# Performance work log

Measured on AMD Instinct MI355X. Metric: run time of the kernel, lower is better.

Reference implementation:

```python
import jax, jax.numpy as jnp
import numpy as np

# static config (matches init_kwargs)
WS = (8, 7, 7)       # window size (T, H, W)
SS = (4, 3, 3)       # shift size (T, H, W)
NUM_HEADS = 4
B, T, H, W, C = 2, 16, 56, 56, 128
VOL = WS[0] * WS[1] * WS[2]  # 392 tokens per window


def _compute_attention_mask_3d(size_dhw, window_size, shift_size):
    """Static numpy replica of torch _compute_attention_mask_3d -> [nW, V, V]."""
    m = np.zeros(size_dhw, dtype=np.float32)
    slices = [((0, -window_size[i]), (-window_size[i], -shift_size[i]), (-shift_size[i], None))
              for i in range(3)]
    cnt = 0
    for d0, d1 in slices[0]:
        for h0, h1 in slices[1]:
            for w0, w1 in slices[2]:
                m[d0:d1, h0:h1, w0:w1] = cnt
                cnt += 1
    nT, nH, nW_ = (size_dhw[0] // window_size[0], size_dhw[1] // window_size[1],
                   size_dhw[2] // window_size[2])
    m = m.reshape(nT, window_size[0], nH, window_size[1], nW_, window_size[2])
    m = m.transpose(0, 2, 4, 1, 3, 5).reshape(nT * nH * nW_, VOL)
    diff = m[:, None, :] - m[:, :, None]
    return np.where(diff != 0, np.float32(-100.0), np.float32(0.0))


_ATTN_MASK = jnp.asarray(_compute_attention_mask_3d((T, H, W), WS, SS))  # [nW, V, V]


def setup_inputs() -> dict:
    key = jax.random.key(0)
    ks = jax.random.split(key, 6)
    s = 0.02
    return {
        "x": jax.random.normal(ks[0], (B, T, H, W, C), jnp.float32),
        "qkv_weight": jax.random.normal(ks[1], (3 * C, C), jnp.float32) * s,
        "qkv_bias": jax.random.normal(ks[2], (3 * C,), jnp.float32) * s,
        "proj_weight": jax.random.normal(ks[3], (C, C), jnp.float32) * s,
        "proj_bias": jax.random.normal(ks[4], (C,), jnp.float32) * s,
        "rel_pos_bias": jax.random.normal(ks[5], (1, NUM_HEADS, VOL, VOL), jnp.float32) * s,
    }


def reference(x, qkv_weight, qkv_bias, proj_weight, proj_bias, rel_pos_bias):
    b, t, h, w, c = x.shape
    hd = c // NUM_HEADS
    wt, wh, ww = WS
    nt, nh, nw = t // wt, h // wh, w // ww
    n_win = nt * nh * nw

    # cyclic shift (T,H,W divide the window so no padding needed)
    xs = jnp.roll(x, shift=(-SS[0], -SS[1], -SS[2]), axis=(1, 2, 3))

    # window partition -> [b*n_win, VOL, c]
    xw = xs.reshape(b, nt, wt, nh, wh, nw, ww, c)
    xw = xw.transpose(0, 1, 3, 5, 2, 4, 6, 7).reshape(b * n_win, VOL, c)

    # qkv projection
    qkv = xw @ qkv_weight.T + qkv_bias
    qkv = qkv.reshape(b * n_win, VOL, 3, NUM_HEADS, hd).transpose(2, 0, 3, 1, 4)
    q, k, v = qkv[0], qkv[1], qkv[2]          # [b*nW, nH, V, hd]
    q = q * (hd ** -0.5)

    attn = jnp.einsum("whqd,whkd->whqk", q, k) + rel_pos_bias
    # shift mask: broadcast over batch and heads
    attn = attn.reshape(b, n_win, NUM_HEADS, VOL, VOL) + _ATTN_MASK[None, :, None, :, :]
    attn = jax.nn.softmax(attn.reshape(b * n_win, NUM_HEADS, VOL, VOL), axis=-1)

    out = jnp.einsum("whqk,whkd->whqd", attn, v)         # [b*nW, nH, V, hd]
    out = out.transpose(0, 2, 1, 3).reshape(b * n_win, VOL, c)
    out = out @ proj_weight.T + proj_bias

    # window un-partition -> [b, t, h, w, c]
    out = out.reshape(b, nt, nh, nw, wt, wh, ww, c)
    out = out.transpose(0, 1, 4, 2, 5, 3, 6, 7).reshape(b, t, h, w, c)
    out = jnp.roll(out, shift=(SS[0], SS[1], SS[2]), axis=(1, 2, 3))
    return out
```

## Files before the change

### kernel.cpp

```cpp
#include <hip/hip_runtime.h>
#include <hip/hip_bf16.h>

typedef __bf16 bf16;
typedef __bf16 bf16x4 __attribute__((ext_vector_type(4)));
typedef __bf16 bf16x8 __attribute__((ext_vector_type(8)));
typedef float f32x4 __attribute__((ext_vector_type(4)));

#define MFMA(a, b, c) __builtin_amdgcn_mfma_f32_16x16x32_bf16(a, b, c, 0, 0, 0)

__device__ inline f32x4 zf4() { return f32x4{0.f, 0.f, 0.f, 0.f}; }

constexpr int Tc = 16, Hc = 56, Wc = 56, Cc = 128, NHc = 4, HDc = 32;
constexpr int VOL = 392;
constexpr int STc = 4, SHc = 3, SWc = 3;
constexpr int TWIN = 256;
constexpr int MTOT = TWIN * VOL;
constexpr int QSZ = TWIN * NHc * VOL * HDc;
constexpr int BMT_N = 8 * 4 * 400 * 416;

__device__ inline bf16x8 zero8() {
    bf16x8 z;
#pragma unroll
    for (int j = 0; j < 8; ++j) z[j] = (bf16)0.0f;
    return z;
}

__device__ inline f32x4 up4(bf16x4 b) {
    f32x4 r;
#pragma unroll
    for (int j = 0; j < 4; ++j) r[j] = (float)b[j];
    return r;
}

__device__ inline int cls_of(int v, int pt, int ph, int pw) {
    int tt = v / 49, rem = v % 49, hh = rem / 7, ww = rem % 7;
    int ct = pt ? (tt < 4 ? 1 : 2) : 0;
    int ch = ph ? (hh < 4 ? 1 : 2) : 0;
    int cw = pw ? (ww < 4 ? 1 : 2) : 0;
    return ct * 9 + ch * 3 + cw;
}

__global__ void prep_kernel(const float* __restrict__ wq, const float* __restrict__ bq,
                            const float* __restrict__ wp, const float* __restrict__ bp,
                            const float* __restrict__ rpb,
                            bf16* __restrict__ wqb, bf16* __restrict__ bqb,
                            bf16* __restrict__ wpb, bf16* __restrict__ bpb,
                            bf16* __restrict__ bmt) {
    const int blk = blockIdx.x, tid = threadIdx.x;
    if (blk < 65) {
        int i = blk * 256 + tid;
        const float* s; bf16* d; int off;
        if (i < 12288)       { s = wq; d = wqb; off = i; }
        else if (i < 12384)  { s = bq; d = bqb; off = i - 12288; }
        else if (i < 16480)  { s = wp; d = wpb; off = i - 12384; }
        else if (i < 16512)  { s = bp; d = bpb; off = i - 16480; }
        else return;
        f32x4 v = *(const f32x4*)(s + (size_t)off * 4);
        bf16x4 o;
#pragma unroll
        for (int j = 0; j < 4; ++j) o[j] = (bf16)v[j];
        *(bf16x4*)(d + (size_t)off * 4) = o;
        return;
    }
    __shared__ unsigned char clsc[392];
    int bb = blk - 65;
    int pat = bb / 100, rem = bb % 100;
    int head = rem / 25, rc = rem % 25;
    int pt = (pat >> 2) & 1, ph = (pat >> 1) & 1, pw = pat & 1;
    for (int v = tid; v < 392; v += 256) clsc[v] = (unsigned char)cls_of(v, pt, ph, pw);
    __syncthreads();
    bf16* dst = bmt + ((size_t)(pat * NHc + head) * 400 + rc * 16) * 416;
    for (int idx = tid; idx < 16 * 104; idx += 256) {
        int lr = idx / 104, c4 = idx % 104;
        int row = rc * 16 + lr;
        bf16x4 o;
        if (row >= VOL) {
#pragma unroll
            for (int j = 0; j < 4; ++j) o[j] = (bf16)0.f;
        } else {
            int rcls = clsc[row];
            const float* brow = rpb + (size_t)(head * VOL + row) * VOL;
#pragma unroll
            for (int j = 0; j < 4; ++j) {
                int col = c4 * 4 + j;
                float v;
                if (col >= VOL) v = -144.0f;
                else {
                    v = brow[col] * 1.4426950408889634f;
                    if (clsc[col] != rcls) v -= 144.0f;
                }
                o[j] = (bf16)v;
            }
        }
        *(bf16x4*)(dst + (size_t)lr * 416 + c4 * 4) = o;
    }
}

__global__ __launch_bounds__(256, 3)
void qkv_kernel(const float* __restrict__ x, const bf16* __restrict__ wq,
                const bf16* __restrict__ bq, bf16* __restrict__ qws,
                bf16* __restrict__ kws, bf16* __restrict__ vws) {
    __shared__ bf16 As[64][136];
    __shared__ bf16 Cs[64][204];
    __shared__ unsigned int rb[64];
    __shared__ unsigned int rbw[64];
    const int tid = threadIdx.x;
    const int m0 = blockIdx.x * 64;

    if (tid < 64) {
        int g = m0 + tid;
        int win = g / VOL, tok = g % VOL;
        int b = win >> 7, wi = win & 127;
        int wt_i = wi >> 6, wh_i = (wi >> 3) & 7, ww_i = wi & 7;
        int tt = tok / 49, r2 = tok % 49, hh = r2 / 7, ww2 = r2 % 7;
        int t = wt_i * 8 + tt + STc; if (t >= Tc) t -= Tc;
        int h = wh_i * 7 + hh + SHc; if (h >= Hc) h -= Hc;
        int w = ww_i * 7 + ww2 + SWc; if (w >= Wc) w -= Wc;
        rb[tid] = (unsigned int)((((b * Tc + t) * Hc + h) * Wc + w) * Cc * 4);
        rbw[tid] = (unsigned int)((win << 9) | tok);
    }
    __syncthreads();

    for (int idx = tid; idx < 64 * 32; idx += 256) {
        int r = idx >> 5, c = idx & 31;
        const float* src = (const float*)((const char*)x + rb[r]) + c * 4;
        f32x4 v = *(const f32x4*)src;
        bf16x4 o;
#pragma unroll
        for (int j = 0; j < 4; ++j) o[j] = (bf16)v[j];
        *(bf16x4*)(&As[r][c * 4]) = o;
    }
    __syncthreads();

    const int wid = tid >> 6, lane = tid & 63;
    const int quad = lane >> 4, l15 = lane & 15;
    const int nbase = wid * 96;

    f32x4 acc[6][4];
#pragma unroll
    for (int mt = 0; mt < 6; ++mt)
#pragma unroll
        for (int nt = 0; nt < 4; ++nt) acc[mt][nt] = zf4();

#pragma unroll
    for (int ko = 0; ko < 4; ++ko) {
        bf16x8 xf[4];
#pragma unroll
        for (int nt = 0; nt < 4; ++nt)
            xf[nt] = *(const bf16x8*)(&As[nt * 16 + l15][ko * 32 + quad * 8]);
#pragma unroll
        for (int mt = 0; mt < 6; ++mt) {
            bf16x8 wf = *(const bf16x8*)(wq + (size_t)(nbase + mt * 16 + l15) * Cc + ko * 32 + quad * 8);
#pragma unroll
            for (int nt = 0; nt < 4; ++nt)
                acc[mt][nt] = MFMA(wf, xf[nt], acc[mt][nt]);
        }
    }

#pragma unroll 1
    for (int phase = 0; phase < 2; ++phase) {
        if ((wid >> 1) == phase) {
#pragma unroll
            for (int mt = 0; mt < 6; ++mt) {
                int colbase = nbase + mt * 16 + quad * 4;
                int lc = colbase - phase * 192;
                bf16x4 bc = *(const bf16x4*)(bq + colbase);
                float scale = (colbase < 128) ? 0.25505653942f : 1.0f;
#pragma unroll
                for (int nt = 0; nt < 4; ++nt) {
                    bf16x4 o;
#pragma unroll
                    for (int r = 0; r < 4; ++r)
                        o[r] = (bf16)((acc[mt][nt][r] + (float)bc[r]) * scale);
                    *(bf16x4*)(&Cs[nt * 16 + l15][lc]) = o;
                }
            }
        }
        __syncthreads();
        for (int u = tid; u < 64 * 6; u += 256) {
            int row = u / 6, s = u - row * 6;
            int gs = phase * 6 + s;
            bf16* basep = (gs < 4) ? qws : (gs < 8) ? kws : vws;
            int head = gs & 3;
            unsigned int p = rbw[row];
            int win = p >> 9, tok = p & 511;
            size_t off = ((size_t)(win * NHc + head) * VOL + tok) * HDc;
#pragma unroll
            for (int c = 0; c < 4; ++c) {
                bf16x4 lo = *(const bf16x4*)(&Cs[row][s * 32 + c * 8]);
                bf16x4 hi = *(const bf16x4*)(&Cs[row][s * 32 + c * 8 + 4]);
                *(bf16x8*)(basep + off + c * 8) = __builtin_shufflevector(lo, hi, 0, 1, 2, 3, 4, 5, 6, 7);
            }
        }
        __syncthreads();
    }
}

__global__ __launch_bounds__(512, 4)
void attn_kernel(const bf16* __restrict__ qws, const bf16* __restrict__ kws,
                 const bf16* __restrict__ vws, const bf16* __restrict__ bmt,
                 bf16* __restrict__ aows) {
    __shared__ bf16 Kl[400][40];
    __shared__ bf16 Vt[32][424];
    __shared__ bf16 Pb[8][2][16][40];

    const int tid = threadIdx.x;
    const int win = blockIdx.x >> 2, head = blockIdx.x & 3;
    const int wi = win & 127;
    const int wt_i = wi >> 6, wh_i = (wi >> 3) & 7, ww_i = wi & 7;
    const int pat = ((wt_i == 1) << 2) | ((wh_i == 7) << 1) | (ww_i == 7);

    const bf16* Qg = qws + (size_t)(win * NHc + head) * VOL * HDc;
    const bf16* Kg = kws + (size_t)(win * NHc + head) * VOL * HDc;
    const bf16* Vg = vws + (size_t)(win * NHc + head) * VOL * HDc;
    const bf16* Bg = bmt + (size_t)(pat * NHc + head) * 400 * 416;

    for (int idx = tid; idx < 400 * 4; idx += 512) {
        int tok = idx >> 2, c = idx & 3;
        bf16x8 v = zero8();
        if (tok < VOL) v = *(const bf16x8*)(Kg + tok * HDc + c * 8);
        *(bf16x8*)(&Kl[tok][c * 8]) = v;
    }
    if (tid < 416) {
        int c = tid & 3, tok4 = (tid >> 2) * 4;
        bf16x8 rr[4];
#pragma unroll
        for (int i = 0; i < 4; ++i)
            rr[i] = (tok4 + i < VOL) ? *(const bf16x8*)(Vg + (tok4 + i) * HDc + c * 8) : zero8();
#pragma unroll
        for (int j = 0; j < 8; ++j) {
            bf16x4 wv;
            wv[0] = rr[0][j]; wv[1] = rr[1][j]; wv[2] = rr[2][j]; wv[3] = rr[3][j];
            *(bf16x4*)(&Vt[c * 8 + j][tok4]) = wv;
        }
    }
    __syncthreads();

    const int wid = tid >> 6, lane = tid & 63;
    const int quad = lane >> 4, l15 = lane & 15;
    bf16* PwA = &Pb[wid][0][0][0];
    bf16* PwB = &Pb[wid][1][0][0];

    for (int pass = 0; pass < 2; ++pass) {
        const int qtA = pass * 16 + wid, qtB = qtA + 8;
        const bool hasB = (qtB < 25);
        const int qbA = qtA * 16, qbB = qtB * 16;
        int qrA = qbA + l15; if (qrA >= VOL) qrA = VOL - 1;
        const bf16x8 qfA = *(const bf16x8*)(Qg + (size_t)qrA * HDc + quad * 8);
        const bf16* BrA = Bg + (size_t)(qbA + l15) * 416;
        const bf16* BrB = BrA;
        bf16x8 qfB;
        if (hasB) {
            int qrB = qbB + l15; if (qrB >= VOL) qrB = VOL - 1;
            qfB = *(const bf16x8*)(Qg + (size_t)qrB * HDc + quad * 8);
            BrB = Bg + (size_t)(qbB + l15) * 416;
        }
        f32x4 oA0 = zf4(), oA1 = zf4(), oB0 = zf4(), oB1 = zf4();
        float lsA = 0.f, lsB = 0.f;
        bf16x4 nbA0 = *(const bf16x4*)(BrA + quad * 4);
        bf16x4 nbA1 = *(const bf16x4*)(BrA + 16 + quad * 4);
        bf16x4 nbB0, nbB1;
        if (hasB) {
            nbB0 = *(const bf16x4*)(BrB + quad * 4);
            nbB1 = *(const bf16x4*)(BrB + 16 + quad * 4);
        }

        bf16x8 kc0 = *(const bf16x8*)(&Kl[l15][quad * 8]);
        bf16x8 kc1 = *(const bf16x8*)(&Kl[16 + l15][quad * 8]);
        bf16x8 vc0 = *(const bf16x8*)(&Vt[l15][quad * 8]);
        bf16x8 vc1 = *(const bf16x8*)(&Vt[16 + l15][quad * 8]);

        auto qk_full = [&](int kb) {
            bf16x8 kn0, kn1;
            if (kb < 384) {
                kn0 = *(const bf16x8*)(&Kl[kb + 32 + l15][quad * 8]);
                kn1 = *(const bf16x8*)(&Kl[kb + 48 + l15][quad * 8]);
            }
            f32x4 cA0 = up4(nbA0), cA1 = up4(nbA1), cB0, cB1;
            if (hasB) { cB0 = up4(nbB0); cB1 = up4(nbB1); }
            if (kb < 384) {
                nbA0 = *(const bf16x4*)(BrA + kb + 32 + quad * 4);
                nbA1 = *(const bf16x4*)(BrA + kb + 48 + quad * 4);
                if (hasB) {
                    nbB0 = *(const bf16x4*)(BrB + kb + 32 + quad * 4);
                    nbB1 = *(const bf16x4*)(BrB + kb + 48 + quad * 4);
                }
            }
            f32x4 sA0 = MFMA(kc0, qfA, cA0);
            f32x4 sA1 = MFMA(kc1, qfA, cA1);
            bf16x4 pA0, pA1;
            float la = 0.f;
#pragma unroll
            for (int r = 0; r < 4; ++r) {
                float e0 = __builtin_amdgcn_exp2f(sA0[r]);
                float e1 = __builtin_amdgcn_exp2f(sA1[r]);
                pA0[r] = (bf16)e0; pA1[r] = (bf16)e1; la += e0 + e1;
            }
            lsA += la;
            *(bf16x4*)(PwA + l15 * 40 + quad * 4) = pA0;
            *(bf16x4*)(PwA + l15 * 40 + 16 + quad * 4) = pA1;
            if (hasB) {
                f32x4 sB0 = MFMA(kc0, qfB, cB0);
                f32x4 sB1 = MFMA(kc1, qfB, cB1);
                bf16x4 pB0, pB1;
                float lb = 0.f;
#pragma unroll
                for (int r = 0; r < 4; ++r) {
                    float e0 = __builtin_amdgcn_exp2f(sB0[r]);
                    float e1 = __builtin_amdgcn_exp2f(sB1[r]);
                    pB0[r] = (bf16)e0; pB1[r] = (bf16)e1; lb += e0 + e1;
                }
                lsB += lb;
                *(bf16x4*)(PwB + l15 * 40 + quad * 4) = pB0;
                *(bf16x4*)(PwB + l15 * 40 + 16 + quad * 4) = pB1;
            }
            kc0 = kn0; kc1 = kn1;
        };
        auto pv = [&](int kb) {
            bf16x8 pfA = *(const bf16x8*)(PwA + l15 * 40 + quad * 8);
            bf16x8 pfB;
            if (hasB) pfB = *(const bf16x8*)(PwB + l15 * 40 + quad * 8);
            bf16x8 vn0, vn1;
            if (kb < 384) {
                vn0 = *(const bf16x8*)(&Vt[l15][kb + 32 + quad * 8]);
                vn1 = *(const bf16x8*)(&Vt[16 + l15][kb + 32 + quad * 8]);
            }
            oA0 = MFMA(vc0, pfA, oA0);
            oA1 = MFMA(vc1, pfA, oA1);
            if (hasB) { oB0 = MFMA(vc0, pfB, oB0); oB1 = MFMA(vc1, pfB, oB1); }
            vc0 = vn0; vc1 = vn1;
        };

        qk_full(0);
#pragma unroll 1
        for (int kt = 1; kt < 12; ++kt) {
            pv((kt - 1) * 32);
            qk_full(kt * 32);
        }
        pv(352);
        {
            f32x4 cA0 = up4(nbA0), cB0;
            if (hasB) cB0 = up4(nbB0);
            f32x4 sA0 = MFMA(kc0, qfA, cA0);
            bf16x4 pA0, z4;
            float la = 0.f;
#pragma unroll
            for (int r = 0; r < 4; ++r) {
                float e0 = __builtin_amdgcn_exp2f(sA0[r]);
                pA0[r] = (bf16)e0; la += e0; z4[r] = (bf16)0.f;
            }
            lsA += la;
            *(bf16x4*)(PwA + l15 * 40 + quad * 4) = pA0;
            *(bf16x4*)(PwA + l15 * 40 + 16 + quad * 4) = z4;
            if (hasB) {
                f32x4 sB0 = MFMA(kc0, qfB, cB0);
                bf16x4 pB0;
                float lb = 0.f;
#pragma unroll
                for (int r = 0; r < 4; ++r) {
                    float e0 = __builtin_amdgcn_exp2f(sB0[r]);
                    pB0[r] = (bf16)e0; lb += e0;
                }
                lsB += lb;
                *(bf16x4*)(PwB + l15 * 40 + quad * 4) = pB0;
                *(bf16x4*)(PwB + l15 * 40 + 16 + quad * 4) = z4;
            }
        }
        pv(384);

        lsA += __shfl_xor(lsA, 16); lsA += __shfl_xor(lsA, 32);
        if (hasB) { lsB += __shfl_xor(lsB, 16); lsB += __shfl_xor(lsB, 32); }
        if (qbA + l15 < VOL) {
            float inv = 1.f / lsA;
            bf16x4 w0, w1;
#pragma unroll
            for (int r = 0; r < 4; ++r) { w0[r] = (bf16)(oA0[r] * inv); w1[r] = (bf16)(oA1[r] * inv); }
            bf16* dst = aows + ((size_t)win * VOL + qbA + l15) * Cc + head * HDc;
            *(bf16x4*)(dst + quad * 4) = w0;
            *(bf16x4*)(dst + 16 + quad * 4) = w1;
        }
        if (hasB && qbB + l15 < VOL) {
            float inv = 1.f / lsB;
            bf16x4 w0, w1;
#pragma unroll
            for (int r = 0; r < 4; ++r) { w0[r] = (bf16)(oB0[r] * inv); w1[r] = (bf16)(oB1[r] * inv); }
            bf16* dst = aows + ((size_t)win * VOL + qbB + l15) * Cc + head * HDc;
            *(bf16x4*)(dst + quad * 4) = w0;
            *(bf16x4*)(dst + 16 + quad * 4) = w1;
        }
    }
}

__global__ __launch_bounds__(256, 2)
void proj_kernel(const bf16* __restrict__ aows, const bf16* __restrict__ wp,
                 const bf16* __restrict__ bp, float* __restrict__ out) {
    __shared__ bf16 As[64][136];
    __shared__ float Csf[64][132];
    __shared__ unsigned int rbo[64];
    const int tid = threadIdx.x;
    const int m0 = blockIdx.x * 64;

    if (tid < 64) {
        int g = m0 + tid;
        int win = g / VOL, tok = g % VOL;
        int b = win >> 7, wi = win & 127;
        int wt_i = wi >> 6, wh_i = (wi >> 3) & 7, ww_i = wi & 7;
        int tt = tok / 49, r2 = tok % 49, hh = r2 / 7, ww2 = r2 % 7;
        int t = wt_i * 8 + tt + STc; if (t >= Tc) t -= Tc;
        int h = wh_i * 7 + hh + SHc; if (h >= Hc) h -= Hc;
        int w = ww_i * 7 + ww2 + SWc; if (w >= Wc) w -= Wc;
        rbo[tid] = (unsigned int)((((b * Tc + t) * Hc + h) * Wc + w) * Cc * 4);
    }
    for (int idx = tid; idx < 64 * 16; idx += 256) {
        int r = idx >> 4, c = idx & 15;
        *(bf16x8*)(&As[r][c * 8]) = *(const bf16x8*)(aows + (size_t)(m0 + r) * Cc + c * 8);
    }
    __syncthreads();

    const int wid = tid >> 6, lane = tid & 63;
    const int quad = lane >> 4, l15 = lane & 15;

    f32x4 acc[8];
#pragma unroll
    for (int mt = 0; mt < 8; ++mt) acc[mt] = zf4();

#pragma unroll
    for (int ko = 0; ko < 4; ++ko) {
        bf16x8 xf = *(const bf16x8*)(&As[wid * 16 + l15][ko * 32 + quad * 8]);
#pragma unroll
        for (int mt = 0; mt < 8; ++mt) {
            bf16x8 wf = *(const bf16x8*)(wp + (size_t)(mt * 16 + l15) * Cc + ko * 32 + quad * 8);
            acc[mt] = MFMA(wf, xf, acc[mt]);
        }
    }
#pragma unroll
    for (int mt = 0; mt < 8; ++mt) {
        int colbase = mt * 16 + quad * 4;
        bf16x4 bc = *(const bf16x4*)(bp + colbase);
        f32x4 o;
#pragma unroll
        for (int r = 0; r < 4; ++r) o[r] = acc[mt][r] + (float)bc[r];
        *(f32x4*)(&Csf[wid * 16 + l15][colbase]) = o;
    }
    __syncthreads();

    for (int idx = tid; idx < 64 * 32; idx += 256) {
        int row = idx >> 5, ch = idx & 31;
        float* dst = (float*)((char*)out + rbo[row]) + ch * 4;
        *(f32x4*)dst = *(const f32x4*)(&Csf[row][ch * 4]);
    }
}

extern "C" void kernel_launch(void* const* d_in, const int* in_sizes, int n_in,
                              void* d_out, int out_size, void* d_ws, size_t ws_size,
                              hipStream_t stream) {
    const float* x    = (const float*)d_in[0];
    const float* wqf  = (const float*)d_in[1];
    const float* bqf  = (const float*)d_in[2];
    const float* wpf  = (const float*)d_in[3];
    const float* bpf  = (const float*)d_in[4];
    const float* rpbf = (const float*)d_in[5];
    float* out = (float*)d_out;

    bf16* wqb  = (bf16*)d_ws;
    bf16* bqb  = wqb + 49152;
    bf16* wpb  = bqb + 384;
    bf16* bpb  = wpb + 16384;
    bf16* bmt  = bpb + 128;
    bf16* qws  = bmt + BMT_N;
    bf16* kws  = qws + QSZ;
    bf16* vws  = kws + QSZ;
    bf16* aows = vws + QSZ;

    hipLaunchKernelGGL(prep_kernel, dim3(865), dim3(256), 0, stream,
                       wqf, bqf, wpf, bpf, rpbf, wqb, bqb, wpb, bpb, bmt);
    hipLaunchKernelGGL(qkv_kernel, dim3(MTOT / 64), dim3(256), 0, stream,
                       x, wqb, bqb, qws, kws, vws);
    hipLaunchKernelGGL(attn_kernel, dim3(TWIN * NHc), dim3(512), 0, stream,
                       qws, kws, vws, bmt, aows);
    hipLaunchKernelGGL(proj_kernel, dim3(MTOT / 64), dim3(256), 0, stream,
                       aows, wpb, bpb, out);
}
```

Baseline: 261.3 us.

## Process all query tiles per wave in one pass sharing K/V fragment loads

The attention kernel used to process query tiles in two passes of up to two tiles each. Each pass reloaded the K and V fragments from shared memory. Now each wave handles three or four query tiles (A, B, C, plus D on wave 0) in a single sweep over the key blocks. Each K/V fragment is loaded once per key block and reused across all the tiles, with QK and PV interleaved through two P buffers. This cuts LDS traffic and loop overhead, but it raises register pressure and puts extra imbalance on wave 0, and it drops the explicit next-block prefetch of K/V.

```diff
diff --git a/kernel.cpp b/kernel.cpp
--- a/kernel.cpp
+++ b/kernel.cpp
@@ -238,157 +238,123 @@
 
     const int wid = tid >> 6, lane = tid & 63;
     const int quad = lane >> 4, l15 = lane & 15;
-    bf16* PwA = &Pb[wid][0][0][0];
-    bf16* PwB = &Pb[wid][1][0][0];
-
-    for (int pass = 0; pass < 2; ++pass) {
-        const int qtA = pass * 16 + wid, qtB = qtA + 8;
-        const bool hasB = (qtB < 25);
-        const int qbA = qtA * 16, qbB = qtB * 16;
-        int qrA = qbA + l15; if (qrA >= VOL) qrA = VOL - 1;
-        const bf16x8 qfA = *(const bf16x8*)(Qg + (size_t)qrA * HDc + quad * 8);
-        const bf16* BrA = Bg + (size_t)(qbA + l15) * 416;
-        const bf16* BrB = BrA;
-        bf16x8 qfB;
-        if (hasB) {
-            int qrB = qbB + l15; if (qrB >= VOL) qrB = VOL - 1;
-            qfB = *(const bf16x8*)(Qg + (size_t)qrB * HDc + quad * 8);
-            BrB = Bg + (size_t)(qbB + l15) * 416;
-        }
-        f32x4 oA0 = zf4(), oA1 = zf4(), oB0 = zf4(), oB1 = zf4();
-        float lsA = 0.f, lsB = 0.f;
-        bf16x4 nbA0 = *(const bf16x4*)(BrA + quad * 4);
-        bf16x4 nbA1 = *(const bf16x4*)(BrA + 16 + quad * 4);
-        bf16x4 nbB0, nbB1;
-        if (hasB) {
-            nbB0 = *(const bf16x4*)(BrB + quad * 4);
-            nbB1 = *(const bf16x4*)(BrB + 16 + quad * 4);
-        }
-
-        bf16x8 kc0 = *(const bf16x8*)(&Kl[l15][quad * 8]);
-        bf16x8 kc1 = *(const bf16x8*)(&Kl[16 + l15][quad * 8]);
-        bf16x8 vc0 = *(const bf16x8*)(&Vt[l15][quad * 8]);
-        bf16x8 vc1 = *(const bf16x8*)(&Vt[16 + l15][quad * 8]);
-
-        auto qk_full = [&](int kb) {
-            bf16x8 kn0, kn1;
-            if (kb < 384) {
-                kn0 = *(const bf16x8*)(&Kl[kb + 32 + l15][quad * 8]);
-                kn1 = *(const bf16x8*)(&Kl[kb + 48 + l15][quad * 8]);
-            }
-            f32x4 cA0 = up4(nbA0), cA1 = up4(nbA1), cB0, cB1;
-            if (hasB) { cB0 = up4(nbB0); cB1 = up4(nbB1); }
-            if (kb < 384) {
-                nbA0 = *(const bf16x4*)(BrA + kb + 32 + quad * 4);
-                nbA1 = *(const bf16x4*)(BrA + kb + 48 + quad * 4);
-                if (hasB) {
-                    nbB0 = *(const bf16x4*)(BrB + kb + 32 + quad * 4);
-                    nbB1 = *(const bf16x4*)(BrB + kb + 48 + quad * 4);
-                }
-            }
-            f32x4 sA0 = MFMA(kc0, qfA, cA0);
-            f32x4 sA1 = MFMA(kc1, qfA, cA1);
-            bf16x4 pA0, pA1;
-            float la = 0.f;
-#pragma unroll
-            for (int r = 0; r < 4; ++r) {
-                float e0 = __builtin_amdgcn_exp2f(sA0[r]);
-                float e1 = __builtin_amdgcn_exp2f(sA1[r]);
-                pA0[r] = (bf16)e0; pA1[r] = (bf16)e1; la += e0 + e1;
-            }
-            lsA += la;
-            *(bf16x4*)(PwA + l15 * 40 + quad * 4) = pA0;
-            *(bf16x4*)(PwA + l15 * 40 + 16 + quad * 4) = pA1;
-            if (hasB) {
-                f32x4 sB0 = MFMA(kc0, qfB, cB0);
-                f32x4 sB1 = MFMA(kc1, qfB, cB1);
-                bf16x4 pB0, pB1;
-                float lb = 0.f;
-#pragma unroll
-                for (int r = 0; r < 4; ++r) {
-                    float e0 = __builtin_amdgcn_exp2f(sB0[r]);
-                    float e1 = __builtin_amdgcn_exp2f(sB1[r]);
-                    pB0[r] = (bf16)e0; pB1[r] = (bf16)e1; lb += e0 + e1;
-                }
-                lsB += lb;
-                *(bf16x4*)(PwB + l15 * 40 + quad * 4) = pB0;
-                *(bf16x4*)(PwB + l15 * 40 + 16 + quad * 4) = pB1;
-            }
-            kc0 = kn0; kc1 = kn1;
-        };
-        auto pv = [&](int kb) {
-            bf16x8 pfA = *(const bf16x8*)(PwA + l15 * 40 + quad * 8);
-            bf16x8 pfB;
-            if (hasB) pfB = *(const bf16x8*)(PwB + l15 * 40 + quad * 8);
-            bf16x8 vn0, vn1;
-            if (kb < 384) {
-                vn0 = *(const bf16x8*)(&Vt[l15][kb + 32 + quad * 8]);
-                vn1 = *(const bf16x8*)(&Vt[16 + l15][kb + 32 + quad * 8]);
-            }
-            oA0 = MFMA(vc0, pfA, oA0);
-            oA1 = MFMA(vc1, pfA, oA1);
-            if (hasB) { oB0 = MFMA(vc0, pfB, oB0); oB1 = MFMA(vc1, pfB, oB1); }
-            vc0 = vn0; vc1 = vn1;
-        };
-
-        qk_full(0);
+    bf16* Pw0 = &Pb[wid][0][0][0];
+    bf16* Pw1 = &Pb[wid][1][0][0];
+    const bool hasD = (wid == 0);
+
+    const int qbA = wid * 16, qbB = qbA + 128, qbC = qbA + 256, qbD = 384;
+    const bf16x8 qfA = *(const bf16x8*)(Qg + (size_t)(qbA + l15) * HDc + quad * 8);
+    const bf16x8 qfB = *(const bf16x8*)(Qg + (size_t)(qbB + l15) * HDc + quad * 8);
+    const bf16x8 qfC = *(const bf16x8*)(Qg + (size_t)(qbC + l15) * HDc + quad * 8);
+    bf16x8 qfD;
+    const int brA = (qbA + l15) * 416, brB = (qbB + l15) * 416;
+    const int brC = (qbC + l15) * 416, brD = (qbD + l15) * 416;
+
+    f32x4 oA0 = zf4(), oA1 = zf4(), oB0 = zf4(), oB1 = zf4();
+    f32x4 oC0 = zf4(), oC1 = zf4(), oD0 = zf4(), oD1 = zf4();
+    float lsA = 0.f, lsB = 0.f, lsC = 0.f, lsD = 0.f;
+
+    bf16x4 nbA0 = *(const bf16x4*)(Bg + brA + quad * 4);
+    bf16x4 nbA1 = *(const bf16x4*)(Bg + brA + 16 + quad * 4);
+    bf16x4 nbB0 = *(const bf16x4*)(Bg + brB + quad * 4);
+    bf16x4 nbB1 = *(const bf16x4*)(Bg + brB + 16 + quad * 4);
+    bf16x4 nbC0 = *(const bf16x4*)(Bg + brC + quad * 4);
+    bf16x4 nbC1 = *(const bf16x4*)(Bg + brC + 16 + quad * 4);
+    bf16x4 nbD0, nbD1;
+    if (hasD) {
+        int qrD = qbD + l15; if (qrD >= VOL) qrD = VOL - 1;
+        qfD = *(const bf16x8*)(Qg + (size_t)qrD * HDc + quad * 8);
+        nbD0 = *(const bf16x4*)(Bg + brD + quad * 4);
+        nbD1 = *(const bf16x4*)(Bg + brD + 16 + quad * 4);
+    }
+
+    auto qk = [&](const bf16x8& kf0, const bf16x8& kf1, const bf16x8& qf,
+                  bf16x4& nb0, bf16x4& nb1, int br, float& ls, bf16* Pw, int kb) {
+        f32x4 c0 = up4(nb0), c1 = up4(nb1);
+        if (kb < 384) {
+            nb0 = *(const bf16x4*)(Bg + br + kb + 32 + quad * 4);
+            nb1 = *(const bf16x4*)(Bg + br + kb + 48 + quad * 4);
+        }
+        f32x4 s0 = MFMA(kf0, qf, c0);
+        f32x4 s1 = MFMA(kf1, qf, c1);
+        bf16x4 p0, p1;
+        float la = 0.f;
+#pragma unroll
+        for (int r = 0; r < 4; ++r) {
+            float e0 = __builtin_amdgcn_exp2f(s0[r]);
+            float e1 = __builtin_amdgcn_exp2f(s1[r]);
+            p0[r] = (bf16)e0; p1[r] = (bf16)e1; la += e0 + e1;
+        }
+        ls += la;
+        *(bf16x4*)(Pw + l15 * 40 + quad * 4) = p0;
+        *(bf16x4*)(Pw + l15 * 40 + 16 + quad * 4) = p1;
+    };
+    auto qkh = [&](const bf16x8& kf0, const bf16x8& qf, bf16x4& nb0, float& ls, bf16* Pw) {
+        f32x4 c0 = up4(nb0);
+        f32x4 s0 = MFMA(kf0, qf, c0);
+        bf16x4 p0, z4;
+        float la = 0.f;
+#pragma unroll
+        for (int r = 0; r < 4; ++r) {
+            float e0 = __builtin_amdgcn_exp2f(s0[r]);
+            p0[r] = (bf16)e0; la += e0; z4[r] = (bf16)0.f;
+        }
+        ls += la;
+        *(bf16x4*)(Pw + l15 * 40 + quad * 4) = p0;
+        *(bf16x4*)(Pw + l15 * 40 + 16 + quad * 4) = z4;
+    };
+    auto pv = [&](bf16* Pw, const bf16x8& vf0, const bf16x8& vf1, f32x4& o0, f32x4& o1) {
+        bf16x8 pf = *(const bf16x8*)(Pw + l15 * 40 + quad * 8);
+        o0 = MFMA(vf0, pf, o0);
+        o1 = MFMA(vf1, pf, o1);
+    };
+
 #pragma unroll 1
-        for (int kt = 1; kt < 12; ++kt) {
-            pv((kt - 1) * 32);
-            qk_full(kt * 32);
-        }
-        pv(352);
-        {
-            f32x4 cA0 = up4(nbA0), cB0;
-            if (hasB) cB0 = up4(nbB0);
-            f32x4 sA0 = MFMA(kc0, qfA, cA0);
-            bf16x4 pA0, z4;
-            float la = 0.f;
-#pragma unroll
-            for (int r = 0; r < 4; ++r) {
-                float e0 = __builtin_amdgcn_exp2f(sA0[r]);
-                pA0[r] = (bf16)e0; la += e0; z4[r] = (bf16)0.f;
-            }
-            lsA += la;
-            *(bf16x4*)(PwA + l15 * 40 + quad * 4) = pA0;
-            *(bf16x4*)(PwA + l15 * 40 + 16 + quad * 4) = z4;
-            if (hasB) {
-                f32x4 sB0 = MFMA(kc0, qfB, cB0);
-                bf16x4 pB0;
-                float lb = 0.f;
-#pragma unroll
-                for (int r = 0; r < 4; ++r) {
-                    float e0 = __builtin_amdgcn_exp2f(sB0[r]);
-                    pB0[r] = (bf16)e0; lb += e0;
-                }
-                lsB += lb;
-                *(bf16x4*)(PwB + l15 * 40 + quad * 4) = pB0;
-                *(bf16x4*)(PwB + l15 * 40 + 16 + quad * 4) = z4;
-            }
-        }
-        pv(384);
-
-        lsA += __shfl_xor(lsA, 16); lsA += __shfl_xor(lsA, 32);
-        if (hasB) { lsB += __shfl_xor(lsB, 16); lsB += __shfl_xor(lsB, 32); }
-        if (qbA + l15 < VOL) {
-            float inv = 1.f / lsA;
+    for (int kt = 0; kt < 12; ++kt) {
+        const int kb = kt * 32;
+        bf16x8 kf0 = *(const bf16x8*)(&Kl[kb + l15][quad * 8]);
+        bf16x8 kf1 = *(const bf16x8*)(&Kl[kb + 16 + l15][quad * 8]);
+        bf16x8 vf0 = *(const bf16x8*)(&Vt[l15][kb + quad * 8]);
+        bf16x8 vf1 = *(const bf16x8*)(&Vt[16 + l15][kb + quad * 8]);
+        qk(kf0, kf1, qfA, nbA0, nbA1, brA, lsA, Pw0, kb);
+        qk(kf0, kf1, qfB, nbB0, nbB1, brB, lsB, Pw1, kb);
+        pv(Pw0, vf0, vf1, oA0, oA1);
+        qk(kf0, kf1, qfC, nbC0, nbC1, brC, lsC, Pw0, kb);
+        pv(Pw1, vf0, vf1, oB0, oB1);
+        if (hasD) qk(kf0, kf1, qfD, nbD0, nbD1, brD, lsD, Pw1, kb);
+        pv(Pw0, vf0, vf1, oC0, oC1);
+        if (hasD) pv(Pw1, vf0, vf1, oD0, oD1);
+    }
+    {
+        bf16x8 kf0 = *(const bf16x8*)(&Kl[384 + l15][quad * 8]);
+        bf16x8 vf0 = *(const bf16x8*)(&Vt[l15][384 + quad * 8]);
+        bf16x8 vf1 = *(const bf16x8*)(&Vt[16 + l15][384 + quad * 8]);
+        qkh(kf0, qfA, nbA0, lsA, Pw0);
+        qkh(kf0, qfB, nbB0, lsB, Pw1);
+        pv(Pw0, vf0, vf1, oA0, oA1);
+        qkh(kf0, qfC, nbC0, lsC, Pw0);
+        pv(Pw1, vf0, vf1, oB0, oB1);
+        if (hasD) qkh(kf0, qfD, nbD0, lsD, Pw1);
+        pv(Pw0, vf0, vf1, oC0, oC1);
+        if (hasD) pv(Pw1, vf0, vf1, oD0, oD1);
+    }
+
+    auto fin = [&](float ls, const f32x4& o0, const f32x4& o1, int qb) {
+        ls += __shfl_xor(ls, 16); ls += __shfl_xor(ls, 32);
+        if (qb + l15 < VOL) {
+            float inv = 1.f / ls;
             bf16x4 w0, w1;
 #pragma unroll
-            for (int r = 0; r < 4; ++r) { w0[r] = (bf16)(oA0[r] * inv); w1[r] = (bf16)(oA1[r] * inv); }
-            bf16* dst = aows + ((size_t)win * VOL + qbA + l15) * Cc + head * HDc;
+            for (int r = 0; r < 4; ++r) { w0[r] = (bf16)(o0[r] * inv); w1[r] = (bf16)(o1[r] * inv); }
+            bf16* dst = aows + ((size_t)win * VOL + qb + l15) * Cc + head * HDc;
             *(bf16x4*)(dst + quad * 4) = w0;
             *(bf16x4*)(dst + 16 + quad * 4) = w1;
         }
-        if (hasB && qbB + l15 < VOL) {
-            float inv = 1.f / lsB;
-            bf16x4 w0, w1;
-#pragma unroll
-            for (int r = 0; r < 4; ++r) { w0[r] = (bf16)(oB0[r] * inv); w1[r] = (bf16)(oB1[r] * inv); }
-            bf16* dst = aows + ((size_t)win * VOL + qbB + l15) * Cc + head * HDc;
-            *(bf16x4*)(dst + quad * 4) = w0;
-            *(bf16x4*)(dst + 16 + quad * 4) = w1;
-        }
-    }
+    };
+    fin(lsA, oA0, oA1, qbA);
+    fin(lsB, oB0, oB1, qbB);
+    fin(lsC, oC0, oC1, qbC);
+    if (hasD) fin(lsD, oD0, oD1, qbD);
 }
 
 __global__ __launch_bounds__(256, 2)
```

New measurement: 277.7 us. 6.3% more time.
